# Optimization experiments

Hardware: AMD Instinct MI355X
Metric: run time of the kernel (lower is better)

## Reference

```python
import jax, jax.numpy as jnp
import numpy as np

DIM = 512
WS = 8
NH = 16
HD = DIM // NH
N = WS * WS
B = 2048
SCALE = HD ** -0.5


def _rel_pos_index(ws):
    # Swin relative position index for a ws x ws window -> [N*N] int indices
    coords = np.stack(np.meshgrid(np.arange(ws), np.arange(ws), indexing='ij')).reshape(2, -1)
    rel = coords[:, :, None] - coords[:, None, :]          # [2, N, N]
    rel = rel.transpose(1, 2, 0).copy()                    # [N, N, 2]
    rel[..., 0] += ws - 1
    rel[..., 1] += ws - 1
    rel[..., 0] *= 2 * ws - 1
    return rel.sum(-1).reshape(-1)                         # [N*N]

REL_IDX = jnp.asarray(_rel_pos_index(WS))


def setup_inputs() -> dict:
    key = jax.random.key(0)
    ks = jax.random.split(key, 6)
    x = jax.random.normal(ks[0], (B, N, DIM), dtype=jnp.float32)
    W_qkv = jax.random.normal(ks[1], (3 * DIM, DIM), dtype=jnp.float32) * 0.02
    b_qkv = jnp.zeros((3 * DIM,), dtype=jnp.float32)
    W_proj = jax.random.normal(ks[2], (DIM, DIM), dtype=jnp.float32) * 0.02
    b_proj = jnp.zeros((DIM,), dtype=jnp.float32)
    bias_table = jax.random.normal(ks[3], ((2 * WS - 1) * (2 * WS - 1), NH), dtype=jnp.float32) * 0.02
    return {"x": x, "W_qkv": W_qkv, "b_qkv": b_qkv, "W_proj": W_proj, "b_proj": b_proj, "bias_table": bias_table}


def reference(x, W_qkv, b_qkv, W_proj, b_proj, bias_table):
    B_, n, c = x.shape
    qkv = x @ W_qkv.T + b_qkv                              # [B, N, 3C]
    qkv = qkv.reshape(B_, n, 3, NH, HD)
    q = qkv[:, :, 0].transpose(0, 2, 1, 3)                 # [B, H, N, hd]
    k = qkv[:, :, 1].transpose(0, 2, 1, 3)
    v = qkv[:, :, 2].transpose(0, 2, 1, 3)
    attn = jnp.einsum('bhnd,bhmd->bhnm', q, k) * SCALE     # [B, H, N, N]
    bias = bias_table[REL_IDX].reshape(n, n, NH).transpose(2, 0, 1)  # [H, N, N]
    attn = jax.nn.softmax(attn + bias[None], axis=-1)
    out = jnp.einsum('bhnm,bhmd->bhnd', attn, v)           # [B, H, N, hd]
    out = out.transpose(0, 2, 1, 3).reshape(B_, n, c)      # [B, N, C]
    return out @ W_proj.T + b_proj
```

## Files before the change

### kernel.cpp

```cpp
#include <hip/hip_runtime.h>
#include <stdint.h>

#define NHEADS 16
#define HDIM 32
#define NTOK 64
#define NWIN_B 2048
#define MROWS (NWIN_B * NTOK)
#define CDIM 512
#define QKVDIM 1536
#define ATT_SCALE 0.17677669529663687f

typedef __attribute__((ext_vector_type(8))) short short8;
typedef __attribute__((ext_vector_type(4))) float f32x4;

__device__ __forceinline__ unsigned short f2bf(float f) {
  unsigned int u = __float_as_uint(f);
  u += 0x7FFFu + ((u >> 16) & 1u);
  return (unsigned short)(u >> 16);
}

__device__ __forceinline__ void gload_lds16(const unsigned short* g, unsigned short* l) {
  __builtin_amdgcn_global_load_lds(
      (const __attribute__((address_space(1))) unsigned int*)g,
      (__attribute__((address_space(3))) unsigned int*)l, 16, 0, 0);
}

__global__ void cvt_bf16_kernel(const float* __restrict__ src,
                                unsigned short* __restrict__ dst, int n4) {
  int i = blockIdx.x * blockDim.x + threadIdx.x;
  if (i >= n4) return;
  const float4 v = ((const float4*)src)[i];
  ushort4 o;
  o.x = f2bf(v.x); o.y = f2bf(v.y); o.z = f2bf(v.z); o.w = f2bf(v.w);
  ((ushort4*)dst)[i] = o;
}

__global__ void expand_bias_kernel(const float* __restrict__ table,
                                   float* __restrict__ biasx) {
  const int t = blockIdx.x * blockDim.x + threadIdx.x;
  const int col = t & 63, row = (t >> 6) & 63, h = t >> 12;
  const int idx = ((row >> 3) - (col >> 3) + 7) * 15 + ((row & 7) - (col & 7) + 7);
  biasx[t] = table[idx * NHEADS + h];
}


#define MMAQ(qm, qn)                                                          \
  do {                                                                        \
    _Pragma("unroll") for (int kk = 0; kk < 2; ++kk)                          \
    _Pragma("unroll") for (int mt = 0; mt < 4; ++mt)                          \
    _Pragma("unroll") for (int nt = 0; nt < 2; ++nt)                          \
      acc[(qm) * 4 + mt][(qn) * 2 + nt] =                                     \
          __builtin_amdgcn_mfma_f32_16x16x32_bf16(                            \
              aF[mt][kk], bF[(qn) * 2 + nt][kk],                              \
              acc[(qm) * 4 + mt][(qn) * 2 + nt], 0, 0, 0);                    \
  } while (0)

#define LDB_Q(buf, qn)                                                        \
  do {                                                                        \
    _Pragma("unroll") for (int nt = 0; nt < 2; ++nt) {                        \
      const int rb_ = wn * 64 + ((qn) * 2 + nt) * 16 + l16;                   \
      _Pragma("unroll") for (int kk = 0; kk < 2; ++kk) {                      \
        const int pb_ = ((kk * 4 + quad) ^ (l16 & 7)) * 8;                    \
        bF[(qn) * 2 + nt][kk] =                                               \
            *(const short8*)&lds[(buf) * BUFSZ + ATILE + rb_ * 64 + pb_];     \
      }                                                                       \
    }                                                                         \
  } while (0)

template <typename OutT>
__global__ __launch_bounds__(512, 2) void gemm256_kernel(
    const unsigned short* __restrict__ A,
    const unsigned short* __restrict__ Bt,
    const float* __restrict__ bias,
    OutT* __restrict__ C, int M, int N, int K, int nxb) {
  constexpr int BK = 64;
  constexpr int ATILE = 256 * BK;
  constexpr int BUFSZ = 2 * ATILE;
  __shared__ __align__(16) unsigned short lds[2 * BUFSZ];

  const int tid = threadIdx.x;
  const int w = tid >> 6, lane = tid & 63;
  const int quad = lane >> 4, l16 = lane & 15;
  const int wm = w >> 2, wn = w & 3;
  const int srow8 = lane >> 3, gch = (lane & 7) ^ srow8;

  const int nyb_per_xcd = (gridDim.x / nxb) >> 3;
  const int xcd = blockIdx.x & 7;
  const int idx = blockIdx.x >> 3;
  const long rowBase = (long)(xcd * nyb_per_xcd + idx / nxb) * 256;
  const long colBase = (long)(idx % nxb) * 256;
  const int NT = K / BK;

  const unsigned short* aSrc = A + (rowBase + w * 8 + srow8) * (long)K + gch * 8;
  const unsigned short* bSrc = Bt + (colBase + w * 8 + srow8) * (long)K + gch * 8;

  auto stageA = [&](int buf, int half, int kt) {
    unsigned short* dst = &lds[buf * BUFSZ + (half * 128 + w * 8) * BK];
    const unsigned short* src = aSrc + (long)half * 128 * K + kt * BK;
    gload_lds16(src, dst);
    gload_lds16(src + 64 * (long)K, dst + 64 * BK);
  };
  auto stageB = [&](int buf, int half, int kt) {
    unsigned short* dst = &lds[buf * BUFSZ + ATILE + (half * 128 + w * 8) * BK];
    const unsigned short* src = bSrc + (long)half * 128 * K + kt * BK;
    gload_lds16(src, dst);
    gload_lds16(src + 64 * (long)K, dst + 64 * BK);
  };

  f32x4 acc[8][4] = {};
  short8 aF[4][2], bF[4][2];

  auto ldA = [&](int buf, int qm) {
#pragma unroll
    for (int mt = 0; mt < 4; ++mt) {
      const int r = wm * 128 + qm * 64 + mt * 16 + l16;
#pragma unroll
      for (int kk = 0; kk < 2; ++kk) {
        const int p = ((kk * 4 + quad) ^ (l16 & 7)) * 8;
        aF[mt][kk] = *(const short8*)&lds[buf * BUFSZ + r * 64 + p];
      }
    }
  };

  stageA(0, 0, 0); stageA(0, 1, 0); stageB(0, 0, 0); stageB(0, 1, 0);
  if (NT > 1) { stageB(1, 0, 1); stageB(1, 1, 1); }
  asm volatile("s_waitcnt vmcnt(4)" ::: "memory");
  __builtin_amdgcn_s_barrier();

  for (int u = 0; u < NT; ++u) {
    const int cur = u & 1, nxt = cur ^ 1;

    ldA(cur, 0);
    LDB_Q(cur, 0);
    if (u + 1 < NT) stageA(nxt, 0, u + 1);
    asm volatile("s_waitcnt lgkmcnt(8)" ::: "memory");
    __builtin_amdgcn_s_barrier();
    asm volatile("s_waitcnt lgkmcnt(0)" ::: "memory");
    __builtin_amdgcn_sched_barrier(0);
    __builtin_amdgcn_s_setprio(1);
    MMAQ(0, 0);
    __builtin_amdgcn_s_setprio(0);
    __builtin_amdgcn_s_barrier();

    LDB_Q(cur, 1);
    if (u + 1 < NT) stageA(nxt, 1, u + 1);
    __builtin_amdgcn_s_barrier();
    asm volatile("s_waitcnt lgkmcnt(0)" ::: "memory");
    __builtin_amdgcn_sched_barrier(0);
    __builtin_amdgcn_s_setprio(1);
    MMAQ(0, 1);
    __builtin_amdgcn_s_setprio(0);
    __builtin_amdgcn_s_barrier();

    ldA(cur, 1);
    if (u + 2 < NT) stageB(cur, 0, u + 2);
    __builtin_amdgcn_s_barrier();
    asm volatile("s_waitcnt lgkmcnt(0)" ::: "memory");
    __builtin_amdgcn_sched_barrier(0);
    __builtin_amdgcn_s_setprio(1);
    MMAQ(1, 1);
    __builtin_amdgcn_s_setprio(0);
    __builtin_amdgcn_s_barrier();

    if (u + 2 < NT) stageB(cur, 1, u + 2);
    __builtin_amdgcn_s_barrier();
    __builtin_amdgcn_s_setprio(1);
    MMAQ(1, 0);
    __builtin_amdgcn_s_setprio(0);
    if (u + 1 < NT) {
      if (u + 2 < NT) asm volatile("s_waitcnt vmcnt(4)" ::: "memory");
      else            asm volatile("s_waitcnt vmcnt(0)" ::: "memory");
    }
    __builtin_amdgcn_s_barrier();
  }

  if constexpr (sizeof(OutT) == 2) {
    unsigned short* Cs = &lds[0];
#pragma unroll
    for (int ni = 0; ni < 4; ++ni) {
      const int col = wn * 64 + ni * 16 + l16;
      const float bv = bias[colBase + col];
#pragma unroll
      for (int mi = 0; mi < 8; ++mi) {
        const int row0 = wm * 128 + mi * 16 + quad * 4;
#pragma unroll
        for (int r = 0; r < 4; ++r)
          Cs[(row0 + r) * 256 + col] = f2bf(acc[mi][ni][r] + bv);
      }
    }
    __syncthreads();
#pragma unroll
    for (int t = 0; t < 16; ++t) {
      const int ci = t * 512 + tid;
      const int row = ci >> 5, ch = ci & 31;
      *(short8*)((unsigned short*)C + (rowBase + row) * N + colBase + ch * 8) =
          *(const short8*)&Cs[ci * 8];
    }
  } else {
#pragma unroll
    for (int ni = 0; ni < 4; ++ni) {
      const long col = colBase + wn * 64 + ni * 16 + l16;
      const float bv = bias[col];
#pragma unroll
      for (int mi = 0; mi < 8; ++mi) {
        const long row0 = rowBase + wm * 128 + mi * 16 + quad * 4;
#pragma unroll
        for (int r = 0; r < 4; ++r)
          C[(row0 + r) * N + col] = acc[mi][ni][r] + bv;
      }
    }
  }
}

__global__ __launch_bounds__(256) void attn_kernel(
    const unsigned short* __restrict__ qkv,
    const float* __restrict__ biasx,
    unsigned short* __restrict__ aout) {
  __shared__ __align__(16) unsigned short sT[3 * 64 * 128];
  unsigned short* P = sT;

  const int tid = threadIdx.x;
  const int w = tid >> 6, lane = tid & 63;
  const int quad = lane >> 4, l16 = lane & 15;
  const int b = blockIdx.x >> 2;
  const int q = blockIdx.x & 3;
  const int h = q * 4 + w;

  const unsigned short* base = qkv + (long)b * NTOK * QKVDIM + q * 128;

  const int rloc = lane >> 4;
  const int ch = lane & 15;
#pragma unroll
  for (int t = 0; t < 3; ++t) {
#pragma unroll
    for (int i = 0; i < 4; ++i) {
      const int r = w * 16 + i * 4 + rloc;
      const int gc = ch ^ (r & 15);
      gload_lds16(base + (long)r * QKVDIM + t * 512 + gc * 8,
                  &sT[t * 8192 + (w * 16 + i * 4) * 128]);
    }
  }
  __syncthreads();

  short8 qF[4], kF[4];
  const int pQ = ((w * 4 + quad) ^ l16) * 8;
#pragma unroll
  for (int t = 0; t < 4; ++t) {
    qF[t] = *(const short8*)&sT[0 * 8192 + (t * 16 + l16) * 128 + pQ];
    kF[t] = *(const short8*)&sT[1 * 8192 + (t * 16 + l16) * 128 + pQ];
  }

  f32x4 S[4][4];
#pragma unroll
  for (int mi = 0; mi < 4; ++mi)
#pragma unroll
    for (int ni = 0; ni < 4; ++ni) {
      f32x4 z = {0.f, 0.f, 0.f, 0.f};
      S[mi][ni] = __builtin_amdgcn_mfma_f32_16x16x32_bf16(qF[mi], kF[ni], z, 0, 0, 0);
    }

  short8 vF[2][2];
#pragma unroll
  for (int kt = 0; kt < 2; ++kt)
#pragma unroll
    for (int dt = 0; dt < 2; ++dt) {
      short8 f;
#pragma unroll
      for (int j = 0; j < 8; ++j) {
        const int n = kt * 32 + quad * 8 + j;
        const int c = w * 4 + dt * 2 + (l16 >> 3);
        f[j] = (short)sT[2 * 8192 + n * 128 + (c ^ (n & 15)) * 8 + (l16 & 7)];
      }
      vF[kt][dt] = f;
    }

  __syncthreads();

  const float* bh = biasx + h * (NTOK * NTOK);
#pragma unroll
  for (int mi = 0; mi < 4; ++mi) {
#pragma unroll
    for (int r = 0; r < 4; ++r) {
      const int row = mi * 16 + quad * 4 + r;
      float vals[4], mx = -3.4e38f;
#pragma unroll
      for (int ni = 0; ni < 4; ++ni) {
        const float s = S[mi][ni][r] * ATT_SCALE + bh[row * 64 + ni * 16 + l16];
        vals[ni] = s;
        mx = fmaxf(mx, s);
      }
#pragma unroll
      for (int d = 1; d < 16; d <<= 1) mx = fmaxf(mx, __shfl_xor(mx, d));
      float sum = 0.f;
#pragma unroll
      for (int ni = 0; ni < 4; ++ni) { vals[ni] = __expf(vals[ni] - mx); sum += vals[ni]; }
#pragma unroll
      for (int d = 1; d < 16; d <<= 1) sum += __shfl_xor(sum, d);
      const float inv = 1.0f / sum;
#pragma unroll
      for (int ni = 0; ni < 4; ++ni)
        P[w * 4608 + row * 72 + ni * 16 + l16] = f2bf(vals[ni] * inv);
    }
  }

  f32x4 O[4][2] = {};
#pragma unroll
  for (int mi = 0; mi < 4; ++mi)
#pragma unroll
    for (int kt = 0; kt < 2; ++kt) {
      const short8 pF = *(const short8*)&P[w * 4608 + (mi * 16 + l16) * 72 + kt * 32 + quad * 8];
#pragma unroll
      for (int dt = 0; dt < 2; ++dt)
        O[mi][dt] = __builtin_amdgcn_mfma_f32_16x16x32_bf16(pF, vF[kt][dt], O[mi][dt], 0, 0, 0);
    }

#pragma unroll
  for (int mi = 0; mi < 4; ++mi)
#pragma unroll
    for (int dt = 0; dt < 2; ++dt)
#pragma unroll
      for (int r = 0; r < 4; ++r) {
        const int row = mi * 16 + quad * 4 + r;
        aout[((long)b * NTOK + row) * CDIM + h * HDIM + dt * 16 + l16] = f2bf(O[mi][dt][r]);
      }
}

extern "C" void kernel_launch(void* const* d_in, const int* in_sizes, int n_in,
                              void* d_out, int out_size, void* d_ws, size_t ws_size,
                              hipStream_t stream) {
  const float* x      = (const float*)d_in[0];
  const float* W_qkv  = (const float*)d_in[1];
  const float* b_qkv  = (const float*)d_in[2];
  const float* W_proj = (const float*)d_in[3];
  const float* b_proj = (const float*)d_in[4];
  const float* btab   = (const float*)d_in[5];

  char* ws = (char*)d_ws;
  unsigned short* qkv   = (unsigned short*)ws;
  unsigned short* xb    = (unsigned short*)(ws + 402653184L);
  unsigned short* aout  = xb;
  unsigned short* wqkvb = (unsigned short*)(ws + 402653184L + 134217728L);
  unsigned short* wprjb = (unsigned short*)(ws + 402653184L + 134217728L + 1572864L);
  float*          biasx = (float*)(ws + 402653184L + 134217728L + 1572864L + 524288L);

  cvt_bf16_kernel<<<(MROWS * CDIM) / 1024, 256, 0, stream>>>(x, xb, (MROWS * CDIM) / 4);
  cvt_bf16_kernel<<<(QKVDIM * CDIM) / 1024, 256, 0, stream>>>(W_qkv, wqkvb, (QKVDIM * CDIM) / 4);
  cvt_bf16_kernel<<<(CDIM * CDIM) / 1024, 256, 0, stream>>>(W_proj, wprjb, (CDIM * CDIM) / 4);
  expand_bias_kernel<<<(NHEADS * NTOK * NTOK) / 256, 256, 0, stream>>>(btab, biasx);

  gemm256_kernel<unsigned short><<<(MROWS / 256) * (QKVDIM / 256), 512, 0, stream>>>(
      xb, wqkvb, b_qkv, qkv, MROWS, QKVDIM, CDIM, QKVDIM / 256);

  attn_kernel<<<NWIN_B * 4, 256, 0, stream>>>(qkv, biasx, aout);

  gemm256_kernel<float><<<(MROWS / 256) * (CDIM / 256), 512, 0, stream>>>(
      aout, wprjb, b_proj, (float*)d_out, MROWS, CDIM, CDIM, CDIM / 256);
}
```

Baseline: 943.8 us.

## Emit V transposed from QKV GEMM and stage attention output through LDS

The QKV GEMM now writes Q and K to a 1024-wide buffer and writes V pre-transposed into per-window, per-head-group slabs. This lets the attention kernel load V^T with vectorized LDS reads instead of gathering scalars element by element. The attention kernel computes O^T = V^T·P^T and stages the result in swizzled LDS, so the output goes out as coalesced 16-byte stores instead of scattered 2-byte stores. In exchange, the GEMM epilogue for V tiles does a strided LDS gather, and the attention kernel gains an extra barrier and an LDS round trip.

```diff
diff --git a/kernel.cpp b/kernel.cpp
--- a/kernel.cpp
+++ b/kernel.cpp
@@ -42,7 +42,6 @@
   const int idx = ((row >> 3) - (col >> 3) + 7) * 15 + ((row & 7) - (col & 7) + 7);
   biasx[t] = table[idx * NHEADS + h];
 }
-
 
 #define MMAQ(qm, qn)                                                          \
   do {                                                                        \
@@ -67,12 +66,61 @@
     }                                                                         \
   } while (0)
 
-template <typename OutT>
-__global__ __launch_bounds__(512, 2) void gemm256_kernel(
+#define GEMM_KLOOP_BODY                                                       \
+  stageA(0, 0, 0); stageA(0, 1, 0); stageB(0, 0, 0); stageB(0, 1, 0);         \
+  if (NT > 1) { stageB(1, 0, 1); stageB(1, 1, 1); }                           \
+  asm volatile("s_waitcnt vmcnt(4)" ::: "memory");                            \
+  __builtin_amdgcn_s_barrier();                                               \
+  for (int u = 0; u < NT; ++u) {                                              \
+    const int cur = u & 1, nxt = cur ^ 1;                                     \
+    ldA(cur, 0);                                                              \
+    LDB_Q(cur, 0);                                                            \
+    if (u + 1 < NT) stageA(nxt, 0, u + 1);                                    \
+    asm volatile("s_waitcnt lgkmcnt(8)" ::: "memory");                        \
+    __builtin_amdgcn_s_barrier();                                             \
+    asm volatile("s_waitcnt lgkmcnt(0)" ::: "memory");                        \
+    __builtin_amdgcn_sched_barrier(0);                                        \
+    __builtin_amdgcn_s_setprio(1);                                            \
+    MMAQ(0, 0);                                                               \
+    __builtin_amdgcn_s_setprio(0);                                            \
+    __builtin_amdgcn_s_barrier();                                             \
+    LDB_Q(cur, 1);                                                            \
+    if (u + 1 < NT) stageA(nxt, 1, u + 1);                                    \
+    __builtin_amdgcn_s_barrier();                                             \
+    asm volatile("s_waitcnt lgkmcnt(0)" ::: "memory");                        \
+    __builtin_amdgcn_sched_barrier(0);                                        \
+    __builtin_amdgcn_s_setprio(1);                                            \
+    MMAQ(0, 1);                                                               \
+    __builtin_amdgcn_s_setprio(0);                                            \
+    __builtin_amdgcn_s_barrier();                                             \
+    ldA(cur, 1);                                                              \
+    if (u + 2 < NT) stageB(cur, 0, u + 2);                                    \
+    __builtin_amdgcn_s_barrier();                                             \
+    asm volatile("s_waitcnt lgkmcnt(0)" ::: "memory");                        \
+    __builtin_amdgcn_sched_barrier(0);                                        \
+    __builtin_amdgcn_s_setprio(1);                                            \
+    MMAQ(1, 1);                                                               \
+    __builtin_amdgcn_s_setprio(0);                                            \
+    __builtin_amdgcn_s_barrier();                                             \
+    if (u + 2 < NT) stageB(cur, 1, u + 2);                                    \
+    __builtin_amdgcn_s_barrier();                                             \
+    __builtin_amdgcn_s_setprio(1);                                            \
+    MMAQ(1, 0);                                                               \
+    __builtin_amdgcn_s_setprio(0);                                            \
+    if (u + 1 < NT) {                                                         \
+      if (u + 2 < NT) asm volatile("s_waitcnt vmcnt(4)" ::: "memory");        \
+      else            asm volatile("s_waitcnt vmcnt(0)" ::: "memory");        \
+    }                                                                         \
+    __builtin_amdgcn_s_barrier();                                             \
+  }
+
+__global__ __launch_bounds__(512, 2) void gemm_qkv_kernel(
     const unsigned short* __restrict__ A,
     const unsigned short* __restrict__ Bt,
     const float* __restrict__ bias,
-    OutT* __restrict__ C, int M, int N, int K, int nxb) {
+    unsigned short* __restrict__ qkOut,
+    unsigned short* __restrict__ vtOut,
+    int M, int K, int nxb) {
   constexpr int BK = 64;
   constexpr int ATILE = 256 * BK;
   constexpr int BUFSZ = 2 * ATILE;
@@ -122,102 +170,128 @@
     }
   };
 
-  stageA(0, 0, 0); stageA(0, 1, 0); stageB(0, 0, 0); stageB(0, 1, 0);
-  if (NT > 1) { stageB(1, 0, 1); stageB(1, 1, 1); }
-  asm volatile("s_waitcnt vmcnt(4)" ::: "memory");
-  __builtin_amdgcn_s_barrier();
-
-  for (int u = 0; u < NT; ++u) {
-    const int cur = u & 1, nxt = cur ^ 1;
-
-    ldA(cur, 0);
-    LDB_Q(cur, 0);
-    if (u + 1 < NT) stageA(nxt, 0, u + 1);
-    asm volatile("s_waitcnt lgkmcnt(8)" ::: "memory");
-    __builtin_amdgcn_s_barrier();
-    asm volatile("s_waitcnt lgkmcnt(0)" ::: "memory");
-    __builtin_amdgcn_sched_barrier(0);
-    __builtin_amdgcn_s_setprio(1);
-    MMAQ(0, 0);
-    __builtin_amdgcn_s_setprio(0);
-    __builtin_amdgcn_s_barrier();
-
-    LDB_Q(cur, 1);
-    if (u + 1 < NT) stageA(nxt, 1, u + 1);
-    __builtin_amdgcn_s_barrier();
-    asm volatile("s_waitcnt lgkmcnt(0)" ::: "memory");
-    __builtin_amdgcn_sched_barrier(0);
-    __builtin_amdgcn_s_setprio(1);
-    MMAQ(0, 1);
-    __builtin_amdgcn_s_setprio(0);
-    __builtin_amdgcn_s_barrier();
-
-    ldA(cur, 1);
-    if (u + 2 < NT) stageB(cur, 0, u + 2);
-    __builtin_amdgcn_s_barrier();
-    asm volatile("s_waitcnt lgkmcnt(0)" ::: "memory");
-    __builtin_amdgcn_sched_barrier(0);
-    __builtin_amdgcn_s_setprio(1);
-    MMAQ(1, 1);
-    __builtin_amdgcn_s_setprio(0);
-    __builtin_amdgcn_s_barrier();
-
-    if (u + 2 < NT) stageB(cur, 1, u + 2);
-    __builtin_amdgcn_s_barrier();
-    __builtin_amdgcn_s_setprio(1);
-    MMAQ(1, 0);
-    __builtin_amdgcn_s_setprio(0);
-    if (u + 1 < NT) {
-      if (u + 2 < NT) asm volatile("s_waitcnt vmcnt(4)" ::: "memory");
-      else            asm volatile("s_waitcnt vmcnt(0)" ::: "memory");
-    }
-    __builtin_amdgcn_s_barrier();
-  }
-
-  if constexpr (sizeof(OutT) == 2) {
-    unsigned short* Cs = &lds[0];
-#pragma unroll
-    for (int ni = 0; ni < 4; ++ni) {
-      const int col = wn * 64 + ni * 16 + l16;
-      const float bv = bias[colBase + col];
-#pragma unroll
-      for (int mi = 0; mi < 8; ++mi) {
-        const int row0 = wm * 128 + mi * 16 + quad * 4;
-#pragma unroll
-        for (int r = 0; r < 4; ++r)
-          Cs[(row0 + r) * 256 + col] = f2bf(acc[mi][ni][r] + bv);
-      }
-    }
-    __syncthreads();
+  GEMM_KLOOP_BODY
+
+  unsigned short* Cs = &lds[0];
+#pragma unroll
+  for (int ni = 0; ni < 4; ++ni) {
+    const int col = wn * 64 + ni * 16 + l16;
+    const float bv = bias[colBase + col];
+#pragma unroll
+    for (int mi = 0; mi < 8; ++mi) {
+      const int row0 = wm * 128 + mi * 16 + quad * 4;
+#pragma unroll
+      for (int r = 0; r < 4; ++r)
+        Cs[(row0 + r) * 256 + col] = f2bf(acc[mi][ni][r] + bv);
+    }
+  }
+  __syncthreads();
+  if (colBase < 1024) {
 #pragma unroll
     for (int t = 0; t < 16; ++t) {
       const int ci = t * 512 + tid;
-      const int row = ci >> 5, ch = ci & 31;
-      *(short8*)((unsigned short*)C + (rowBase + row) * N + colBase + ch * 8) =
+      const int row = ci >> 5, ch2 = ci & 31;
+      *(short8*)(qkOut + (rowBase + row) * 1024 + colBase + ch2 * 8) =
           *(const short8*)&Cs[ci * 8];
     }
   } else {
-#pragma unroll
-    for (int ni = 0; ni < 4; ++ni) {
-      const long col = colBase + wn * 64 + ni * 16 + l16;
-      const float bv = bias[col];
-#pragma unroll
-      for (int mi = 0; mi < 8; ++mi) {
-        const long row0 = rowBase + wm * 128 + mi * 16 + quad * 4;
-#pragma unroll
-        for (int r = 0; r < 4; ++r)
-          C[(row0 + r) * N + col] = acc[mi][ni][r] + bv;
+    const int qpair = (int)((colBase - 1024) >> 7);
+#pragma unroll
+    for (int t = 0; t < 16; ++t) {
+      const int ci = t * 512 + tid;
+      const int d = ci & 127;
+      const int k0 = (ci >> 7) & 7;
+      const int slabi = ci >> 10;
+      const int winloc = slabi >> 1, qsel = slabi & 1;
+      short8 v;
+#pragma unroll
+      for (int j = 0; j < 8; ++j)
+        v[j] = (short)Cs[(winloc * 64 + k0 * 8 + j) * 256 + qsel * 128 + d];
+      const long slab = ((rowBase >> 6) + winloc) * 4 + qpair + qsel;
+      *(short8*)(vtOut + slab * 8192 + (long)d * 64 + k0 * 8) = v;
+    }
+  }
+}
+
+__global__ __launch_bounds__(512, 2) void gemm256_kernel(
+    const unsigned short* __restrict__ A,
+    const unsigned short* __restrict__ Bt,
+    const float* __restrict__ bias,
+    float* __restrict__ C, int M, int N, int K, int nxb) {
+  constexpr int BK = 64;
+  constexpr int ATILE = 256 * BK;
+  constexpr int BUFSZ = 2 * ATILE;
+  __shared__ __align__(16) unsigned short lds[2 * BUFSZ];
+
+  const int tid = threadIdx.x;
+  const int w = tid >> 6, lane = tid & 63;
+  const int quad = lane >> 4, l16 = lane & 15;
+  const int wm = w >> 2, wn = w & 3;
+  const int srow8 = lane >> 3, gch = (lane & 7) ^ srow8;
+
+  const int nyb_per_xcd = (gridDim.x / nxb) >> 3;
+  const int xcd = blockIdx.x & 7;
+  const int idx = blockIdx.x >> 3;
+  const long rowBase = (long)(xcd * nyb_per_xcd + idx / nxb) * 256;
+  const long colBase = (long)(idx % nxb) * 256;
+  const int NT = K / BK;
+
+  const unsigned short* aSrc = A + (rowBase + w * 8 + srow8) * (long)K + gch * 8;
+  const unsigned short* bSrc = Bt + (colBase + w * 8 + srow8) * (long)K + gch * 8;
+
+  auto stageA = [&](int buf, int half, int kt) {
+    unsigned short* dst = &lds[buf * BUFSZ + (half * 128 + w * 8) * BK];
+    const unsigned short* src = aSrc + (long)half * 128 * K + kt * BK;
+    gload_lds16(src, dst);
+    gload_lds16(src + 64 * (long)K, dst + 64 * BK);
+  };
+  auto stageB = [&](int buf, int half, int kt) {
+    unsigned short* dst = &lds[buf * BUFSZ + ATILE + (half * 128 + w * 8) * BK];
+    const unsigned short* src = bSrc + (long)half * 128 * K + kt * BK;
+    gload_lds16(src, dst);
+    gload_lds16(src + 64 * (long)K, dst + 64 * BK);
+  };
+
+  f32x4 acc[8][4] = {};
+  short8 aF[4][2], bF[4][2];
+
+  auto ldA = [&](int buf, int qm) {
+#pragma unroll
+    for (int mt = 0; mt < 4; ++mt) {
+      const int r = wm * 128 + qm * 64 + mt * 16 + l16;
+#pragma unroll
+      for (int kk = 0; kk < 2; ++kk) {
+        const int p = ((kk * 4 + quad) ^ (l16 & 7)) * 8;
+        aF[mt][kk] = *(const short8*)&lds[buf * BUFSZ + r * 64 + p];
       }
     }
+  };
+
+  GEMM_KLOOP_BODY
+
+#pragma unroll
+  for (int ni = 0; ni < 4; ++ni) {
+    const long col = colBase + wn * 64 + ni * 16 + l16;
+    const float bv = bias[col];
+#pragma unroll
+    for (int mi = 0; mi < 8; ++mi) {
+      const long row0 = rowBase + wm * 128 + mi * 16 + quad * 4;
+#pragma unroll
+      for (int r = 0; r < 4; ++r)
+        C[(row0 + r) * N + col] = acc[mi][ni][r] + bv;
+    }
   }
 }
 
 __global__ __launch_bounds__(256) void attn_kernel(
-    const unsigned short* __restrict__ qkv,
+    const unsigned short* __restrict__ qk,
+    const unsigned short* __restrict__ vtg,
     const float* __restrict__ biasx,
     unsigned short* __restrict__ aout) {
-  __shared__ __align__(16) unsigned short sT[3 * 64 * 128];
-  unsigned short* P = sT;
+  __shared__ __align__(16) unsigned short sm[26624];
+  unsigned short* P  = sm;
+  unsigned short* Vt = sm + 18432;
+  unsigned short* Ot = sm + 18432;
 
   const int tid = threadIdx.x;
   const int w = tid >> 6, lane = tid & 63;
@@ -226,18 +300,24 @@
   const int q = blockIdx.x & 3;
   const int h = q * 4 + w;
 
-  const unsigned short* base = qkv + (long)b * NTOK * QKVDIM + q * 128;
-
-  const int rloc = lane >> 4;
-  const int ch = lane & 15;
-#pragma unroll
-  for (int t = 0; t < 3; ++t) {
+  const int rloc = lane >> 4, ch = lane & 15;
+#pragma unroll
+  for (int t = 0; t < 2; ++t)
 #pragma unroll
     for (int i = 0; i < 4; ++i) {
       const int r = w * 16 + i * 4 + rloc;
       const int gc = ch ^ (r & 15);
-      gload_lds16(base + (long)r * QKVDIM + t * 512 + gc * 8,
-                  &sT[t * 8192 + (w * 16 + i * 4) * 128]);
+      gload_lds16(qk + (long)(b * 64 + r) * 1024 + t * 512 + q * 128 + gc * 8,
+                  &sm[t * 8192 + (w * 16 + i * 4) * 128]);
+    }
+  {
+    const int dloc = lane >> 3, pos = lane & 7;
+#pragma unroll
+    for (int i = 0; i < 4; ++i) {
+      const int d = w * 32 + i * 8 + dloc;
+      const int gc = pos ^ (d & 7);
+      gload_lds16(vtg + (long)(b * 4 + q) * 8192 + (long)d * 64 + gc * 8,
+                  &Vt[(w * 32 + i * 8) * 64]);
     }
   }
   __syncthreads();
@@ -246,8 +326,8 @@
   const int pQ = ((w * 4 + quad) ^ l16) * 8;
 #pragma unroll
   for (int t = 0; t < 4; ++t) {
-    qF[t] = *(const short8*)&sT[0 * 8192 + (t * 16 + l16) * 128 + pQ];
-    kF[t] = *(const short8*)&sT[1 * 8192 + (t * 16 + l16) * 128 + pQ];
+    qF[t] = *(const short8*)&sm[0 * 8192 + (t * 16 + l16) * 128 + pQ];
+    kF[t] = *(const short8*)&sm[1 * 8192 + (t * 16 + l16) * 128 + pQ];
   }
 
   f32x4 S[4][4];
@@ -259,19 +339,14 @@
       S[mi][ni] = __builtin_amdgcn_mfma_f32_16x16x32_bf16(qF[mi], kF[ni], z, 0, 0, 0);
     }
 
-  short8 vF[2][2];
-#pragma unroll
-  for (int kt = 0; kt < 2; ++kt)
-#pragma unroll
-    for (int dt = 0; dt < 2; ++dt) {
-      short8 f;
-#pragma unroll
-      for (int j = 0; j < 8; ++j) {
-        const int n = kt * 32 + quad * 8 + j;
-        const int c = w * 4 + dt * 2 + (l16 >> 3);
-        f[j] = (short)sT[2 * 8192 + n * 128 + (c ^ (n & 15)) * 8 + (l16 & 7)];
-      }
-      vF[kt][dt] = f;
+  short8 vA[2][2];
+#pragma unroll
+  for (int dt = 0; dt < 2; ++dt)
+#pragma unroll
+    for (int kt = 0; kt < 2; ++kt) {
+      const int dl = w * 32 + dt * 16 + l16;
+      const int p = (((kt * 4 + quad) ^ (dl & 7))) * 8;
+      vA[dt][kt] = *(const short8*)&Vt[dl * 64 + p];
     }
 
   __syncthreads();
@@ -303,26 +378,42 @@
     }
   }
 
-  f32x4 O[4][2] = {};
-#pragma unroll
-  for (int mi = 0; mi < 4; ++mi)
+  f32x4 acc2[2][4] = {};
+#pragma unroll
+  for (int rt = 0; rt < 4; ++rt)
 #pragma unroll
     for (int kt = 0; kt < 2; ++kt) {
-      const short8 pF = *(const short8*)&P[w * 4608 + (mi * 16 + l16) * 72 + kt * 32 + quad * 8];
+      const short8 pF =
+          *(const short8*)&P[w * 4608 + (rt * 16 + l16) * 72 + kt * 32 + quad * 8];
 #pragma unroll
       for (int dt = 0; dt < 2; ++dt)
-        O[mi][dt] = __builtin_amdgcn_mfma_f32_16x16x32_bf16(pF, vF[kt][dt], O[mi][dt], 0, 0, 0);
-    }
-
-#pragma unroll
-  for (int mi = 0; mi < 4; ++mi)
-#pragma unroll
-    for (int dt = 0; dt < 2; ++dt)
-#pragma unroll
-      for (int r = 0; r < 4; ++r) {
-        const int row = mi * 16 + quad * 4 + r;
-        aout[((long)b * NTOK + row) * CDIM + h * HDIM + dt * 16 + l16] = f2bf(O[mi][dt][r]);
+        acc2[dt][rt] = __builtin_amdgcn_mfma_f32_16x16x32_bf16(
+            vA[dt][kt], pF, acc2[dt][rt], 0, 0, 0);
+    }
+
+  __syncthreads();
+
+#pragma unroll
+  for (int dt = 0; dt < 2; ++dt)
+#pragma unroll
+    for (int rt = 0; rt < 4; ++rt)
+#pragma unroll
+      for (int rg = 0; rg < 4; ++rg) {
+        const int r = rt * 16 + l16;
+        const int c = w * 32 + dt * 16 + quad * 4 + rg;
+        const int pos = (c >> 3) ^ (r & 15);
+        Ot[r * 128 + pos * 8 + (c & 7)] = f2bf(acc2[dt][rt][rg]);
       }
+  __syncthreads();
+
+#pragma unroll
+  for (int it = 0; it < 4; ++it) {
+    const int ci = it * 256 + tid;
+    const int row = ci >> 4, p = ci & 15;
+    const short8 v = *(const short8*)&Ot[row * 128 + p * 8];
+    const int c8 = p ^ (row & 15);
+    *(short8*)(aout + (long)(b * 64 + row) * 512 + q * 128 + c8 * 8) = v;
+  }
 }
 
 extern "C" void kernel_launch(void* const* d_in, const int* in_sizes, int n_in,
@@ -336,23 +427,24 @@
   const float* btab   = (const float*)d_in[5];
 
   char* ws = (char*)d_ws;
-  unsigned short* qkv   = (unsigned short*)ws;
+  unsigned short* qk    = (unsigned short*)ws;
+  unsigned short* vt    = (unsigned short*)(ws + 268435456L);
   unsigned short* xb    = (unsigned short*)(ws + 402653184L);
   unsigned short* aout  = xb;
-  unsigned short* wqkvb = (unsigned short*)(ws + 402653184L + 134217728L);
-  unsigned short* wprjb = (unsigned short*)(ws + 402653184L + 134217728L + 1572864L);
-  float*          biasx = (float*)(ws + 402653184L + 134217728L + 1572864L + 524288L);
+  unsigned short* wqkvb = (unsigned short*)(ws + 536870912L);
+  unsigned short* wprjb = (unsigned short*)(ws + 536870912L + 1572864L);
+  float*          biasx = (float*)(ws + 536870912L + 1572864L + 524288L);
 
   cvt_bf16_kernel<<<(MROWS * CDIM) / 1024, 256, 0, stream>>>(x, xb, (MROWS * CDIM) / 4);
   cvt_bf16_kernel<<<(QKVDIM * CDIM) / 1024, 256, 0, stream>>>(W_qkv, wqkvb, (QKVDIM * CDIM) / 4);
   cvt_bf16_kernel<<<(CDIM * CDIM) / 1024, 256, 0, stream>>>(W_proj, wprjb, (CDIM * CDIM) / 4);
   expand_bias_kernel<<<(NHEADS * NTOK * NTOK) / 256, 256, 0, stream>>>(btab, biasx);
 
-  gemm256_kernel<unsigned short><<<(MROWS / 256) * (QKVDIM / 256), 512, 0, stream>>>(
-      xb, wqkvb, b_qkv, qkv, MROWS, QKVDIM, CDIM, QKVDIM / 256);
-
-  attn_kernel<<<NWIN_B * 4, 256, 0, stream>>>(qkv, biasx, aout);
-
-  gemm256_kernel<float><<<(MROWS / 256) * (CDIM / 256), 512, 0, stream>>>(
+  gemm_qkv_kernel<<<(MROWS / 256) * (QKVDIM / 256), 512, 0, stream>>>(
+      xb, wqkvb, b_qkv, qk, vt, MROWS, CDIM, QKVDIM / 256);
+
+  attn_kernel<<<NWIN_B * 4, 256, 0, stream>>>(qk, vt, biasx, aout);
+
+  gemm256_kernel<<<(MROWS / 256) * (CDIM / 256), 512, 0, stream>>>(
       aout, wprjb, b_proj, (float*)d_out, MROWS, CDIM, CDIM, CDIM / 256);
 }
```

Measured after the change: 949.7 us. Within noise of the previous version (+0.6%).
